# Kernel optimization log

Measured on AMD Instinct MI355X. Metric: run time of the kernel, lower is better.

The kernel has to match this reference:

```python
import jax, jax.numpy as jnp
import numpy as np

EPS = 1e-5

def conv2d(x, w, b=None, pad=1):
    # x: [B,C,H,W], w: [O,I,kh,kw]
    y = jax.lax.conv_general_dilated(x, w, (1, 1), [(pad, pad), (pad, pad)],
                                     dimension_numbers=('NCHW', 'OIHW', 'NCHW'))
    if b is not None:
        y = y + b[None, :, None, None]
    return y

def bn(x, g, b, m, v):
    # inference-mode batchnorm
    inv = g / jnp.sqrt(v + EPS)
    return x * inv[None, :, None, None] + (b - m * inv)[None, :, None, None]

def coord_conv(x, w, b):
    B, C, H, W = x.shape
    yy = jnp.broadcast_to(jnp.linspace(-1.0, 1.0, H)[:, None], (H, W))
    xx = jnp.broadcast_to(jnp.linspace(-1.0, 1.0, W)[None, :], (H, W))
    coords = jnp.broadcast_to(jnp.stack([xx, yy])[None], (B, 2, H, W)).astype(x.dtype)
    return conv2d(jnp.concatenate([x, coords], axis=1), w, b, pad=1)

def deform_conv(x, offset, w):
    # deformable conv v1, 3x3, pad=1, stride=1, no bias
    B, C, H, W = x.shape
    K = 9
    # offset channels interleaved (y, x) per kernel tap
    off = offset.reshape(B, K, 2, H, W)
    off_y, off_x = off[:, :, 0], off[:, :, 1]          # [B,9,H,W]
    k = jnp.arange(K)
    ko_y = (k // 3 - 1).astype(x.dtype)[None, :, None, None]
    ko_x = (k % 3 - 1).astype(x.dtype)[None, :, None, None]
    base_y = jnp.arange(H, dtype=x.dtype)[None, None, :, None]
    base_x = jnp.arange(W, dtype=x.dtype)[None, None, None, :]
    py = base_y + ko_y + off_y                          # [B,9,H,W]
    px = base_x + ko_x + off_x
    xf = x.reshape(B, C, H * W)
    y0 = jnp.floor(py)
    x0 = jnp.floor(px)
    acc = jnp.zeros((B, C, K, H, W), x.dtype)
    for dy in (0.0, 1.0):
        for dx in (0.0, 1.0):
            yy = y0 + dy
            xx = x0 + dx
            wgt = (1.0 - jnp.abs(py - yy)) * (1.0 - jnp.abs(px - xx))
            valid = (yy >= 0) & (yy < H) & (xx >= 0) & (xx < W)
            wgt = jnp.where(valid, wgt, 0.0)            # zero padding OOB
            yi = jnp.clip(yy, 0, H - 1).astype(jnp.int32)
            xi = jnp.clip(xx, 0, W - 1).astype(jnp.int32)
            idx = (yi * W + xi).reshape(B, K * H * W)
            v = jnp.take_along_axis(xf, idx[:, None, :], axis=2).reshape(B, C, K, H, W)
            acc = acc + v * wgt[:, None]
    wk = w.reshape(w.shape[0], w.shape[1], K)           # [O,I,9]
    return jnp.einsum('bckhw,ock->bohw', acc, wk)

def setup_inputs() -> dict:
    key = jax.random.key(0)
    ks = jax.random.split(key, 16)
    d_model, hd = 256, 64
    B, H, W = 8, 96, 96
    f32 = jnp.float32
    def bn_params(k):
        k1, k2, k3 = jax.random.split(k, 3)
        return (1.0 + 0.1 * jax.random.normal(k1, (hd,), f32),
                0.1 * jax.random.normal(k2, (hd,), f32),
                0.1 * jax.random.normal(k3, (hd,), f32),
                0.5 + jax.random.uniform(jax.random.fold_in(k, 7), (hd,), f32))
    bn1 = bn_params(ks[1]); bn2 = bn_params(ks[2]); bn3 = bn_params(ks[3]); bn4 = bn_params(ks[4])
    inp = {
        'features': jax.random.normal(ks[0], (B, H, W, d_model), f32),
        'coord_w': 0.05 * jax.random.normal(ks[5], (hd, d_model + 2, 3, 3), f32),
        'coord_b': jnp.zeros((hd,), f32),
        'bn1_g': bn1[0], 'bn1_b': bn1[1], 'bn1_m': bn1[2], 'bn1_v': bn1[3],
        'off_w': 0.01 * jax.random.normal(ks[6], (18, hd, 3, 3), f32),
        'off_b': 0.01 * jax.random.normal(ks[7], (18,), f32),
        'dc_w': 0.05 * jax.random.normal(ks[8], (hd, hd, 3, 3), f32),
        'bn2_g': bn2[0], 'bn2_b': bn2[1], 'bn2_m': bn2[2], 'bn2_v': bn2[3],
        'r1_w': 0.05 * jax.random.normal(ks[9], (hd, hd, 3, 3), f32),
        'bn3_g': bn3[0], 'bn3_b': bn3[1], 'bn3_m': bn3[2], 'bn3_v': bn3[3],
        'r2_w': 0.05 * jax.random.normal(ks[10], (hd, hd, 3, 3), f32),
        'bn4_g': bn4[0], 'bn4_b': bn4[1], 'bn4_m': bn4[2], 'bn4_v': bn4[3],
        'out_w': 0.1 * jax.random.normal(ks[11], (1, hd, 1, 1), f32),
        'out_b': jnp.zeros((1,), f32),
    }
    return inp

def reference(features, coord_w, coord_b, bn1_g, bn1_b, bn1_m, bn1_v,
              off_w, off_b, dc_w, bn2_g, bn2_b, bn2_m, bn2_v,
              r1_w, bn3_g, bn3_b, bn3_m, bn3_v,
              r2_w, bn4_g, bn4_b, bn4_m, bn4_v, out_w, out_b):
    x = jnp.transpose(features, (0, 3, 1, 2))           # NHWC -> NCHW
    x = jax.nn.relu(bn(coord_conv(x, coord_w, coord_b), bn1_g, bn1_b, bn1_m, bn1_v))
    offset = conv2d(x, off_w, off_b, pad=1)
    x = deform_conv(x, offset, dc_w)
    x = jax.nn.relu(bn(x, bn2_g, bn2_b, bn2_m, bn2_v))
    x = jax.nn.relu(bn(conv2d(x, r1_w, None, pad=1), bn3_g, bn3_b, bn3_m, bn3_v))
    x = jax.nn.relu(bn(conv2d(x, r2_w, None, pad=1), bn4_g, bn4_b, bn4_m, bn4_v))
    return jax.nn.sigmoid(conv2d(x, out_w, out_b, pad=0))
```

## Files before the change

kernel.cpp:

```cpp
#include <hip/hip_runtime.h>


typedef unsigned short u16;
typedef unsigned int u32;
typedef __attribute__((ext_vector_type(8)))  short bf16x8;
typedef __attribute__((ext_vector_type(16))) float f32x16;

#define EPSBN 1e-5f

__device__ __forceinline__ u16 f2bf(float f) {
  u32 u = __builtin_bit_cast(u32, f);
  u32 r = u + 0x7FFFu + ((u >> 16) & 1u);
  return (u16)(r >> 16);
}
__device__ __forceinline__ u32 pk2(float a, float b) {
  return (u32)f2bf(a) | ((u32)f2bf(b) << 16);
}
__device__ __forceinline__ float lo2f(u32 w) { return __builtin_bit_cast(float, w << 16); }
__device__ __forceinline__ float hi2f(u32 w) { return __builtin_bit_cast(float, w & 0xFFFF0000u); }

#define O_X1   0u
#define O_X0B  9437184u
#define O_X2   9437184u
#define O_X3   18874368u
#define O_OFF  47185920u
#define O_PRE  52494336u
#define O_WCF  54853632u
#define O_WOF  55148544u
#define O_WDF  55222272u
#define O_WR1  55296000u
#define O_WR2  55369728u

#define N_X0G 2359296
#define N_WCF 147456
#define N_WOF 36864
#define N_W64 36864
#define N_PRE 589824
#define N_TOT (N_X0G + N_WCF + N_WOF + 3*N_W64 + N_PRE)

__global__ __launch_bounds__(256) void prep_kernel(
    const float* __restrict__ feat,
    const float* __restrict__ coord_w, const float* __restrict__ coord_b,
    const float* __restrict__ off_w, const float* __restrict__ dc_w,
    const float* __restrict__ r1_w, const float* __restrict__ r2_w,
    u16* __restrict__ x0b,
    u16* __restrict__ wcf, u16* __restrict__ wof, u16* __restrict__ wdf,
    u16* __restrict__ wr1, u16* __restrict__ wr2, float* __restrict__ pre)
{
  for (int i = blockIdx.x * 256 + threadIdx.x; i < N_TOT;
       i += gridDim.x * 256) {
    int d = i;
    if (d < N_X0G) {
      const float* p = feat + (size_t)d * 8;
      const float4 f0 = *(const float4*)p;
      const float4 f1 = *(const float4*)(p + 4);
      uint4 o = {pk2(f0.x, f0.y), pk2(f0.z, f0.w),
                 pk2(f1.x, f1.y), pk2(f1.z, f1.w)};
      ((uint4*)x0b)[d] = o;
      continue;
    }
    d -= N_X0G;
    if (d < N_WCF) {
      int j = d & 7, lane = (d >> 3) & 63, frag = d >> 9;
      int nt = frag & 1, h = (frag >> 1) & 3, tap = (frag >> 3) % 9, cc = (frag >> 3) / 9;
      int ic = cc * 64 + h * 16 + ((lane >> 5) << 3) + j;
      int oc = nt * 32 + (lane & 31);
      wcf[d] = f2bf(coord_w[((size_t)oc * 258 + ic) * 9 + tap]);
      continue;
    }
    d -= N_WCF;
    if (d < N_WOF) {
      int j = d & 7, lane = (d >> 3) & 63, frag = d >> 9;
      int nt = frag & 1, h = (frag >> 1) & 3, tap = frag >> 3;
      int ic = h * 16 + ((lane >> 5) << 3) + j;
      int oc = lane & 31;
      wof[d] = (nt == 0 && oc < 18)
                   ? f2bf(off_w[((size_t)oc * 64 + ic) * 9 + tap]) : (u16)0;
      continue;
    }
    d -= N_WOF;
    if (d < 3 * N_W64) {
      int seg = d / N_W64;
      int e = d - seg * N_W64;
      int j = e & 7, lane = (e >> 3) & 63, frag = e >> 9;
      int nt = frag & 1, h = (frag >> 1) & 3, tap = frag >> 3;
      int ic = h * 16 + ((lane >> 5) << 3) + j;
      int oc = nt * 32 + (lane & 31);
      const float* src = (seg == 0) ? dc_w : (seg == 1) ? r1_w : r2_w;
      u16* dst = (seg == 0) ? wdf : (seg == 1) ? wr1 : wr2;
      dst[e] = f2bf(src[((size_t)oc * 64 + ic) * 9 + tap]);
      continue;
    }
    d -= 3 * N_W64;
    int oc = d & 63;
    int r = d >> 6;
    int x = r % 96, y = r / 96;
    float s = coord_b[oc];
    #pragma unroll
    for (int tap = 0; tap < 9; ++tap) {
      const int dy = tap / 3, dx = tap - dy * 3;
      const int sy = y + dy - 1, sx = x + dx - 1;
      if ((unsigned)sy < 96u && (unsigned)sx < 96u) {
        const float xx = -1.f + (2.f / 95.f) * (float)sx;
        const float yy = -1.f + (2.f / 95.f) * (float)sy;
        s += coord_w[((size_t)oc * 258 + 256) * 9 + tap] * xx
           + coord_w[((size_t)oc * 258 + 257) * 9 + tap] * yy;
      }
    }
    pre[((size_t)(y * 96 + x) << 6) + oc] = s;
  }
}

__global__ __launch_bounds__(512, 4) void coord_conv_kernel(
    const u16* __restrict__ x0b, const u16* __restrict__ wcf,
    const float* __restrict__ pre,
    const float* __restrict__ g, const float* __restrict__ bb,
    const float* __restrict__ m, const float* __restrict__ v,
    u16* __restrict__ x1b)
{
  __shared__ __align__(16) u16 buf[2][204 * 72];
  const int t = threadIdx.x;
  const int wv = t >> 6, lane = t & 63;
  const int l31 = lane & 31, l5 = lane >> 5;
  const int row = wv >> 1, nt = wv & 1;
  const int x0 = blockIdx.x * 32, y0 = blockIdx.y * 4, b = blockIdx.z;

  int rpx[4], rgg[4]; size_t rgo[4]; bool rok[4], ract[4];
  #pragma unroll
  for (int it = 0; it < 4; ++it) {
    int r = t + it * 512;
    ract[it] = (r < 1632);
    int px = r >> 3; if (px > 203) px = 203;
    rgg[it] = r & 7;
    rpx[it] = px;
    int ly = px / 34, lx = px - ly * 34;
    int gy = y0 + ly - 1, gx = x0 + lx - 1;
    rok[it] = ract[it] && ((unsigned)gy < 96u) && ((unsigned)gx < 96u);
    rgo[it] = (((size_t)((b * 96 + gy) * 96 + gx)) << 8) + rgg[it] * 8;
  }

  uint4 ra[4];
  #pragma unroll
  for (int it = 0; it < 4; ++it) {
    ra[it] = make_uint4(0u, 0u, 0u, 0u);
    if (rok[it]) ra[it] = *(const uint4*)(x0b + rgo[it]);
  }
  #pragma unroll
  for (int it = 0; it < 4; ++it) if (ract[it])
    *(uint4*)(&buf[0][rpx[it] * 72 + rgg[it] * 8]) = ra[it];
  __syncthreads();

  f32x16 acc = {};
  for (int cc = 0; cc < 4; ++cc) {
    const int cur = cc & 1;
    if (cc < 3) {
      #pragma unroll
      for (int it = 0; it < 4; ++it) {
        ra[it] = make_uint4(0u, 0u, 0u, 0u);
        if (rok[it]) ra[it] = *(const uint4*)(x0b + rgo[it] + (cc + 1) * 64);
      }
    }
    #pragma unroll
    for (int tap = 0; tap < 9; ++tap) {
      const int dy = tap / 3, dx = tap - dy * 3;
      #pragma unroll
      for (int h = 0; h < 4; ++h) {
        const bf16x8 afr = *(const bf16x8*)(
            &buf[cur][((row + dy) * 34 + l31 + dx) * 72 + h * 16 + l5 * 8]);
        const bf16x8 bfr = *(const bf16x8*)(
            wcf + ((size_t)(((cc * 9 + tap) * 4 + h) * 2 + nt)) * 512 + lane * 8);
        acc = __builtin_amdgcn_mfma_f32_32x32x16_bf16(afr, bfr, acc, 0, 0, 0);
      }
    }
    if (cc < 3) {
      #pragma unroll
      for (int it = 0; it < 4; ++it) if (ract[it])
        *(uint4*)(&buf[1 - cur][rpx[it] * 72 + rgg[it] * 8]) = ra[it];
    }
    __syncthreads();
  }

  const int oc = nt * 32 + l31;
  const float inv = g[oc] * rsqrtf(v[oc] + EPSBN);
  const float sh = bb[oc] - m[oc] * inv;
  const int y = y0 + row;
  #pragma unroll
  for (int r = 0; r < 16; ++r) {
    const int xr = (r & 3) + 8 * (r >> 2) + 4 * l5;
    const int x = x0 + xr;
    const float pv = pre[((size_t)(y * 96 + x) << 6) + oc];
    const float val = fmaxf(fmaf(acc[r] + pv, inv, sh), 0.f);
    x1b[(((size_t)((b * 96 + y) * 96 + x)) << 6) + oc] = f2bf(val);
  }
}

template<int EPI>
__global__ __launch_bounds__(512, 4) void conv64_kernel(
    const u16* __restrict__ xin, const u16* __restrict__ wf,
    const float* __restrict__ g, const float* __restrict__ bb,
    const float* __restrict__ m, const float* __restrict__ v,
    const float* __restrict__ ow, const float* __restrict__ ob,
    void* __restrict__ outp)
{
  __shared__ __align__(16) u16 tile[204 * 72];
  __shared__ float red[128];
  const int t = threadIdx.x;
  const int wv = t >> 6, lane = t & 63;
  const int l31 = lane & 31, l5 = lane >> 5;
  const int row = wv >> 1, nt = wv & 1;
  const int x0 = blockIdx.x * 32, y0 = blockIdx.y * 4, b = blockIdx.z;

  if constexpr (EPI == 2) { if (t < 128) red[t] = 0.f; }

  #pragma unroll
  for (int it = 0; it < 4; ++it) {
    int r = t + it * 512;
    if (r < 1632) {
      int px = r >> 3, gg = r & 7;
      int ly = px / 34, lx = px - ly * 34;
      int gy = y0 + ly - 1, gx = x0 + lx - 1;
      uint4 o = {0u, 0u, 0u, 0u};
      if ((unsigned)gy < 96u && (unsigned)gx < 96u)
        o = *(const uint4*)(xin + (((size_t)((b * 96 + gy) * 96 + gx)) << 6)
                            + gg * 8);
      *(uint4*)(&tile[px * 72 + gg * 8]) = o;
    }
  }
  __syncthreads();

  f32x16 acc = {};
  #pragma unroll
  for (int tap = 0; tap < 9; ++tap) {
    const int dy = tap / 3, dx = tap - dy * 3;
    #pragma unroll
    for (int h = 0; h < 4; ++h) {
      const bf16x8 afr = *(const bf16x8*)(
          &tile[((row + dy) * 34 + l31 + dx) * 72 + h * 16 + l5 * 8]);
      const bf16x8 bfr = *(const bf16x8*)(
          wf + ((size_t)((tap * 4 + h) * 2 + nt)) * 512 + lane * 8);
      acc = __builtin_amdgcn_mfma_f32_32x32x16_bf16(afr, bfr, acc, 0, 0, 0);
    }
  }

  const int y = y0 + row;
  if constexpr (EPI == 1) {
    if (nt == 0 && l31 < 18) {
      float* fo = (float*)outp;
      const float bs = ow[l31];
      #pragma unroll
      for (int r = 0; r < 16; ++r) {
        const int xr = (r & 3) + 8 * (r >> 2) + 4 * l5;
        fo[((size_t)((b * 96 + y) * 96 + x0 + xr)) * 18 + l31] = acc[r] + bs;
      }
    }
    return;
  }

  const int oc = nt * 32 + l31;
  const float inv = g[oc] * rsqrtf(v[oc] + EPSBN);
  const float sh = bb[oc] - m[oc] * inv;

  if constexpr (EPI == 0) {
    u16* xo = (u16*)outp;
    #pragma unroll
    for (int r = 0; r < 16; ++r) {
      const int xr = (r & 3) + 8 * (r >> 2) + 4 * l5;
      const float val = fmaxf(fmaf(acc[r], inv, sh), 0.f);
      xo[(((size_t)((b * 96 + y) * 96 + x0 + xr)) << 6) + oc] = f2bf(val);
    }
  } else if constexpr (EPI == 2) {
    const float wo = ow[oc];
    float pr[16];
    #pragma unroll
    for (int r = 0; r < 16; ++r)
      pr[r] = fmaxf(fmaf(acc[r], inv, sh), 0.f) * wo;
    #pragma unroll
    for (int mask = 1; mask <= 16; mask <<= 1)
      #pragma unroll
      for (int r = 0; r < 16; ++r)
        pr[r] += __shfl_xor(pr[r], mask);
    if (l31 == 0) {
      #pragma unroll
      for (int r = 0; r < 16; ++r) {
        const int xr = (r & 3) + 8 * (r >> 2) + 4 * l5;
        atomicAdd(&red[row * 32 + xr], pr[r]);
      }
    }
    __syncthreads();
    if (t < 128) {
      float* fo = (float*)outp;
      const int yy = y0 + (t >> 5), xx = x0 + (t & 31);
      const float val = red[t] + ob[0];
      fo[(size_t)(b * 96 + yy) * 96 + xx] = 1.f / (1.f + expf(-val));
    }
  }
}

__global__ __launch_bounds__(256, 4) void deform_kernel(
    const u16* __restrict__ x1b, const float* __restrict__ off,
    const u16* __restrict__ wdf,
    const float* __restrict__ g, const float* __restrict__ bb,
    const float* __restrict__ m, const float* __restrict__ v,
    u16* __restrict__ x2b)
{
  __shared__ float offs[128 * 18];
  const int t = threadIdx.x;
  const int wv = t >> 6, lane = t & 63;
  const int l31 = lane & 31, l5 = lane >> 5;
  const int x0 = blockIdx.x * 16, y0 = blockIdx.y * 8, b = blockIdx.z;

  for (int i = t; i < 2304; i += 256) {
    const int p = i / 18, c = i - p * 18;
    const int gy = y0 + (p >> 4), gx = x0 + (p & 15);
    offs[i] = off[((size_t)((b * 96 + gy) * 96 + gx)) * 18 + c];
  }
  __syncthreads();

  const int pa = wv * 32 + l31;
  const int pay = y0 + (pa >> 4), pax = x0 + (pa & 15);

  f32x16 acc0 = {}, acc1 = {};

  for (int k = 0; k < 9; ++k) {
    const int kdy = k / 3, kdx = k - kdy * 3;
    const float oy = offs[pa * 18 + 2 * k];
    const float ox = offs[pa * 18 + 2 * k + 1];
    const float py = (float)(pay + kdy - 1) + oy;
    const float px = (float)(pax + kdx - 1) + ox;
    const float yf = floorf(py), xf = floorf(px);
    const float fy = py - yf, fx = px - xf;
    const int yi = (int)yf, xi = (int)xf;

    const u16* base[4];
    float cw[4];
    #pragma unroll
    for (int cor = 0; cor < 4; ++cor) {
      const int cy = yi + (cor >> 1), cx = xi + (cor & 1);
      const bool okc = ((unsigned)cy < 96u) && ((unsigned)cx < 96u);
      const float wy = (cor & 2) ? fy : 1.f - fy;
      const float wx = (cor & 1) ? fx : 1.f - fx;
      cw[cor] = okc ? wy * wx : 0.f;
      const int cyc = cy < 0 ? 0 : (cy > 95 ? 95 : cy);
      const int cxc = cx < 0 ? 0 : (cx > 95 ? 95 : cx);
      base[cor] = x1b + (((size_t)((b * 96 + cyc) * 96 + cxc)) << 6);
    }

    #pragma unroll
    for (int h = 0; h < 4; ++h) {
      const int chg = h * 16 + l5 * 8;
      uint4 cv[4];
      #pragma unroll
      for (int cor = 0; cor < 4; ++cor)
        cv[cor] = *(const uint4*)(base[cor] + chg);
      float o8[8];
      #pragma unroll
      for (int u = 0; u < 8; ++u) o8[u] = 0.f;
      #pragma unroll
      for (int cor = 0; cor < 4; ++cor) {
        const float wgt = cw[cor];
        const u32 uu[4] = {cv[cor].x, cv[cor].y, cv[cor].z, cv[cor].w};
        #pragma unroll
        for (int u = 0; u < 4; ++u) {
          o8[2 * u]     = fmaf(wgt, lo2f(uu[u]), o8[2 * u]);
          o8[2 * u + 1] = fmaf(wgt, hi2f(uu[u]), o8[2 * u + 1]);
        }
      }
      u32 pkd[4];
      #pragma unroll
      for (int u = 0; u < 4; ++u) pkd[u] = pk2(o8[2 * u], o8[2 * u + 1]);
      bf16x8 afr;
      #pragma unroll
      for (int u = 0; u < 4; ++u) {
        afr[2 * u]     = (short)(pkd[u] & 0xFFFFu);
        afr[2 * u + 1] = (short)(pkd[u] >> 16);
      }
      const bf16x8 bf0 = *(const bf16x8*)(
          wdf + ((size_t)((k * 4 + h) * 2 + 0)) * 512 + lane * 8);
      const bf16x8 bf1 = *(const bf16x8*)(
          wdf + ((size_t)((k * 4 + h) * 2 + 1)) * 512 + lane * 8);
      acc0 = __builtin_amdgcn_mfma_f32_32x32x16_bf16(afr, bf0, acc0, 0, 0, 0);
      acc1 = __builtin_amdgcn_mfma_f32_32x32x16_bf16(afr, bf1, acc1, 0, 0, 0);
    }
  }

  #pragma unroll
  for (int nt = 0; nt < 2; ++nt) {
    const int oc = nt * 32 + l31;
    const float inv = g[oc] * rsqrtf(v[oc] + EPSBN);
    const float sh = bb[oc] - m[oc] * inv;
    const f32x16& a = nt ? acc1 : acc0;
    #pragma unroll
    for (int r = 0; r < 16; ++r) {
      const int p = wv * 32 + (r & 3) + 8 * (r >> 2) + 4 * l5;
      const int y = y0 + (p >> 4), x = x0 + (p & 15);
      const float val = fmaxf(fmaf(a[r], inv, sh), 0.f);
      x2b[(((size_t)((b * 96 + y) * 96 + x)) << 6) + oc] = f2bf(val);
    }
  }
}

extern "C" void kernel_launch(void* const* d_in, const int* in_sizes, int n_in,
                              void* d_out, int out_size, void* d_ws,
                              size_t ws_size, hipStream_t stream)
{
  (void)in_sizes; (void)n_in; (void)out_size; (void)ws_size;
  const float* features = (const float*)d_in[0];
  const float* coord_w  = (const float*)d_in[1];
  const float* coord_b  = (const float*)d_in[2];
  const float* bn1g = (const float*)d_in[3];
  const float* bn1b = (const float*)d_in[4];
  const float* bn1m = (const float*)d_in[5];
  const float* bn1v = (const float*)d_in[6];
  const float* off_w = (const float*)d_in[7];
  const float* off_b = (const float*)d_in[8];
  const float* dc_w  = (const float*)d_in[9];
  const float* bn2g = (const float*)d_in[10];
  const float* bn2b = (const float*)d_in[11];
  const float* bn2m = (const float*)d_in[12];
  const float* bn2v = (const float*)d_in[13];
  const float* r1_w = (const float*)d_in[14];
  const float* bn3g = (const float*)d_in[15];
  const float* bn3b = (const float*)d_in[16];
  const float* bn3m = (const float*)d_in[17];
  const float* bn3v = (const float*)d_in[18];
  const float* r2_w = (const float*)d_in[19];
  const float* bn4g = (const float*)d_in[20];
  const float* bn4b = (const float*)d_in[21];
  const float* bn4m = (const float*)d_in[22];
  const float* bn4v = (const float*)d_in[23];
  const float* out_w = (const float*)d_in[24];
  const float* out_b = (const float*)d_in[25];

  char* W = (char*)d_ws;
  u16*   x1b = (u16*)(W + O_X1);
  u16*   x0b = (u16*)(W + O_X0B);
  u16*   x2b = (u16*)(W + O_X2);
  u16*   x3b = (u16*)(W + O_X3);
  float* offb = (float*)(W + O_OFF);
  float* pre = (float*)(W + O_PRE);
  u16*   wcf = (u16*)(W + O_WCF);
  u16*   wof = (u16*)(W + O_WOF);
  u16*   wdf = (u16*)(W + O_WDF);
  u16*   wr1 = (u16*)(W + O_WR1);
  u16*   wr2 = (u16*)(W + O_WR2);

  prep_kernel<<<2048, 256, 0, stream>>>(
      features, coord_w, coord_b, off_w, dc_w, r1_w, r2_w, x0b,
      wcf, wof, wdf, wr1, wr2, pre);

  dim3 grid(3, 24, 8);
  dim3 gridD(6, 12, 8);

  coord_conv_kernel<<<grid, 512, 0, stream>>>(
      x0b, wcf, pre, bn1g, bn1b, bn1m, bn1v, x1b);
  conv64_kernel<1><<<grid, 512, 0, stream>>>(
      x1b, wof, nullptr, nullptr, nullptr, nullptr, off_b, nullptr,
      (void*)offb);
  deform_kernel<<<gridD, 256, 0, stream>>>(
      x1b, offb, wdf, bn2g, bn2b, bn2m, bn2v, x2b);
  conv64_kernel<0><<<grid, 512, 0, stream>>>(
      x2b, wr1, bn3g, bn3b, bn3m, bn3v, nullptr, nullptr, (void*)x3b);
  conv64_kernel<2><<<grid, 512, 0, stream>>>(
      x3b, wr2, bn4g, bn4b, bn4m, bn4v, out_w, out_b, d_out);
}
```

Baseline: 298.5 us.

## Add dedicated offset-conv kernel and split deform K across waves

The offset conv no longer runs through the generic 64-channel conv kernel with a wasted second N-tile. It now has its own 256-thread kernel that computes only the first 32 output channels, 18 of them real. The deform kernel moves to 512 threads: two wave groups each handle half of the channel chunks for the same pixel tile, and their partial MFMA accumulators are summed through shared memory before the BN/ReLU epilogue. The goal is to drop redundant MFMA work in the offset conv and double the parallelism that hides gather latency in the deform conv. The cost is an extra LDS reduction with a barrier, and half the waves sit idle during the epilogue.

```diff
diff --git a/kernel.cpp b/kernel.cpp
--- a/kernel.cpp
+++ b/kernel.cpp
@@ -243,19 +243,6 @@
   }
 
   const int y = y0 + row;
-  if constexpr (EPI == 1) {
-    if (nt == 0 && l31 < 18) {
-      float* fo = (float*)outp;
-      const float bs = ow[l31];
-      #pragma unroll
-      for (int r = 0; r < 16; ++r) {
-        const int xr = (r & 3) + 8 * (r >> 2) + 4 * l5;
-        fo[((size_t)((b * 96 + y) * 96 + x0 + xr)) * 18 + l31] = acc[r] + bs;
-      }
-    }
-    return;
-  }
-
   const int oc = nt * 32 + l31;
   const float inv = g[oc] * rsqrtf(v[oc] + EPSBN);
   const float sh = bb[oc] - m[oc] * inv;
@@ -296,27 +283,80 @@
   }
 }
 
-__global__ __launch_bounds__(256, 4) void deform_kernel(
+__global__ __launch_bounds__(256, 4) void offconv_kernel(
+    const u16* __restrict__ xin, const u16* __restrict__ wf,
+    const float* __restrict__ ob_, float* __restrict__ outp)
+{
+  __shared__ __align__(16) u16 tile[204 * 72];
+  const int t = threadIdx.x;
+  const int wv = t >> 6, lane = t & 63;
+  const int l31 = lane & 31, l5 = lane >> 5;
+  const int x0 = blockIdx.x * 32, y0 = blockIdx.y * 4, b = blockIdx.z;
+
+  #pragma unroll
+  for (int it = 0; it < 7; ++it) {
+    int r = t + it * 256;
+    if (r < 1632) {
+      int px = r >> 3, gg = r & 7;
+      int ly = px / 34, lx = px - ly * 34;
+      int gy = y0 + ly - 1, gx = x0 + lx - 1;
+      uint4 o = {0u, 0u, 0u, 0u};
+      if ((unsigned)gy < 96u && (unsigned)gx < 96u)
+        o = *(const uint4*)(xin + (((size_t)((b * 96 + gy) * 96 + gx)) << 6)
+                            + gg * 8);
+      *(uint4*)(&tile[px * 72 + gg * 8]) = o;
+    }
+  }
+  __syncthreads();
+
+  f32x16 acc = {};
+  #pragma unroll
+  for (int tap = 0; tap < 9; ++tap) {
+    const int dy = tap / 3, dx = tap - dy * 3;
+    #pragma unroll
+    for (int h = 0; h < 4; ++h) {
+      const bf16x8 afr = *(const bf16x8*)(
+          &tile[((wv + dy) * 34 + l31 + dx) * 72 + h * 16 + l5 * 8]);
+      const bf16x8 bfr = *(const bf16x8*)(
+          wf + ((size_t)((tap * 4 + h) * 2 + 0)) * 512 + lane * 8);
+      acc = __builtin_amdgcn_mfma_f32_32x32x16_bf16(afr, bfr, acc, 0, 0, 0);
+    }
+  }
+
+  if (l31 < 18) {
+    const int y = y0 + wv;
+    const float bs = ob_[l31];
+    #pragma unroll
+    for (int r = 0; r < 16; ++r) {
+      const int xr = (r & 3) + 8 * (r >> 2) + 4 * l5;
+      outp[((size_t)((b * 96 + y) * 96 + x0 + xr)) * 18 + l31] = acc[r] + bs;
+    }
+  }
+}
+
+__global__ __launch_bounds__(512, 2) void deform_kernel(
     const u16* __restrict__ x1b, const float* __restrict__ off,
     const u16* __restrict__ wdf,
     const float* __restrict__ g, const float* __restrict__ bb,
     const float* __restrict__ m, const float* __restrict__ v,
     u16* __restrict__ x2b)
 {
-  __shared__ float offs[128 * 18];
+  __shared__ float arena[8192];
   const int t = threadIdx.x;
   const int wv = t >> 6, lane = t & 63;
   const int l31 = lane & 31, l5 = lane >> 5;
+  const int mtile = wv & 3, khalf = wv >> 2;
   const int x0 = blockIdx.x * 16, y0 = blockIdx.y * 8, b = blockIdx.z;
 
-  for (int i = t; i < 2304; i += 256) {
+  float* offs = arena;
+  for (int i = t; i < 2304; i += 512) {
     const int p = i / 18, c = i - p * 18;
     const int gy = y0 + (p >> 4), gx = x0 + (p & 15);
     offs[i] = off[((size_t)((b * 96 + gy) * 96 + gx)) * 18 + c];
   }
   __syncthreads();
 
-  const int pa = wv * 32 + l31;
+  const int pa = mtile * 32 + l31;
   const int pay = y0 + (pa >> 4), pax = x0 + (pa & 15);
 
   f32x16 acc0 = {}, acc1 = {};
@@ -346,7 +386,8 @@
     }
 
     #pragma unroll
-    for (int h = 0; h < 4; ++h) {
+    for (int hh = 0; hh < 2; ++hh) {
+      const int h = khalf * 2 + hh;
       const int chg = h * 16 + l5 * 8;
       uint4 cv[4];
       #pragma unroll
@@ -383,18 +424,35 @@
     }
   }
 
-  #pragma unroll
-  for (int nt = 0; nt < 2; ++nt) {
-    const int oc = nt * 32 + l31;
-    const float inv = g[oc] * rsqrtf(v[oc] + EPSBN);
-    const float sh = bb[oc] - m[oc] * inv;
-    const f32x16& a = nt ? acc1 : acc0;
+  __syncthreads();
+  float* red = arena + (size_t)mtile * 2048;
+  if (khalf == 1) {
     #pragma unroll
     for (int r = 0; r < 16; ++r) {
-      const int p = wv * 32 + (r & 3) + 8 * (r >> 2) + 4 * l5;
-      const int y = y0 + (p >> 4), x = x0 + (p & 15);
-      const float val = fmaxf(fmaf(a[r], inv, sh), 0.f);
-      x2b[(((size_t)((b * 96 + y) * 96 + x)) << 6) + oc] = f2bf(val);
+      red[r * 64 + lane]        = acc0[r];
+      red[(16 + r) * 64 + lane] = acc1[r];
+    }
+  }
+  __syncthreads();
+  if (khalf == 0) {
+    #pragma unroll
+    for (int r = 0; r < 16; ++r) {
+      acc0[r] += red[r * 64 + lane];
+      acc1[r] += red[(16 + r) * 64 + lane];
+    }
+    #pragma unroll
+    for (int nt = 0; nt < 2; ++nt) {
+      const int oc = nt * 32 + l31;
+      const float inv = g[oc] * rsqrtf(v[oc] + EPSBN);
+      const float sh = bb[oc] - m[oc] * inv;
+      const f32x16& a = nt ? acc1 : acc0;
+      #pragma unroll
+      for (int r = 0; r < 16; ++r) {
+        const int p = mtile * 32 + (r & 3) + 8 * (r >> 2) + 4 * l5;
+        const int y = y0 + (p >> 4), x = x0 + (p & 15);
+        const float val = fmaxf(fmaf(a[r], inv, sh), 0.f);
+        x2b[(((size_t)((b * 96 + y) * 96 + x)) << 6) + oc] = f2bf(val);
+      }
     }
   }
 }
@@ -453,10 +511,8 @@
 
   coord_conv_kernel<<<grid, 512, 0, stream>>>(
       x0b, wcf, pre, bn1g, bn1b, bn1m, bn1v, x1b);
-  conv64_kernel<1><<<grid, 512, 0, stream>>>(
-      x1b, wof, nullptr, nullptr, nullptr, nullptr, off_b, nullptr,
-      (void*)offb);
-  deform_kernel<<<gridD, 256, 0, stream>>>(
+  offconv_kernel<<<grid, 256, 0, stream>>>(x1b, wof, off_b, offb);
+  deform_kernel<<<gridD, 512, 0, stream>>>(
       x1b, offb, wdf, bn2g, bn2b, bn2m, bn2v, x2b);
   conv64_kernel<0><<<grid, 512, 0, stream>>>(
       x2b, wr1, bn3g, bn3b, bn3m, bn3v, nullptr, nullptr, (void*)x3b);
```

Result: no change. 301.0 us (+0.8%).
